# Performance work log

Measured on AMD Instinct MI355X. Metric: run time of the kernel, lower is better.

The kernel has to match this reference:

```python
import jax, jax.numpy as jnp
import numpy as np


def setup_inputs() -> dict:
    key = jax.random.key(0)
    k1, k2 = jax.random.split(key)
    batch, cw_dim = 4096, 1024
    dim_embedding, book_size = 8, 256
    dim_codes = cw_dim // dim_embedding  # 128
    x = jax.random.normal(k1, (batch, cw_dim), dtype=jnp.float32)
    codebook = jax.random.normal(k2, (dim_codes, book_size, dim_embedding), dtype=jnp.float32)
    return {"x": x, "codebook": codebook}


def reference(x, codebook):
    # Faithful JAX version of VQVAE.quantise:
    #   pairwise squared distance -> argmin -> gather embeddings -> one-hot scatter
    C, K, D = codebook.shape          # dim_codes, book_size, dim_embedding
    B = x.shape[0]
    xr = x.reshape(B, C, D)           # [B, C, D] (= view(batch*dim_codes, 1, D))
    x2 = jnp.sum(xr * xr, axis=-1)                       # [B, C]
    c2 = jnp.sum(codebook * codebook, axis=-1)           # [C, K]
    dist = x2[..., None] - 2.0 * jnp.einsum('bcd,ckd->bck', xr, codebook) + c2[None]
    idx = jnp.argmin(dist, axis=-1)                      # [B, C]
    # gather nearest codebook entry per code slot
    cw_embed = codebook[jnp.arange(C)[None, :], idx]     # [B, C, D]
    cw_embed = cw_embed.reshape(B, C * D)                # [B, cw_dim]
    # one-hot scatter of selected indices
    one_hot_idx = jax.nn.one_hot(idx, K, dtype=jnp.float32)  # [B, C, K]
    return cw_embed, one_hot_idx
```

## Files before the change

### kernel.cpp

```cpp
#include <hip/hip_runtime.h>


constexpr int B_  = 4096;
constexpr int C_  = 128;
constexpr int K_  = 256;
constexpr int D_  = 8;
constexpr int TPB = 256;

constexpr int   BPT   = 4;
constexpr int   BTILE = TPB * BPT;
constexpr float TAU2  = 1.0e-3f;

typedef float vf4 __attribute__((ext_vector_type(4)));

__device__ __forceinline__ void repair_amb(
    const float xfj[D_], int& k1j, const float s1j, const float s2j,
    const float* s_cbf, const int lane)
{
    const bool amb = (s2j - s1j) <= TAU2;
    unsigned long long mask = __ballot(amb);
    while (mask) {
        const int src = (int)__ffsll((long long)mask) - 1;
        mask &= mask - 1;
        double xd[D_];
        #pragma unroll
        for (int d = 0; d < D_; ++d) xd[d] = (double)__shfl(xfj[d], src);
        double best = 1.0e300;
        int    bk   = 0;
        #pragma unroll
        for (int t = 0; t < 4; ++t) {
            const int k = lane * 4 + t;
            const float* cv = s_cbf + k * D_;
            double cd[D_];
            #pragma unroll
            for (int d = 0; d < D_; ++d) cd[d] = (double)cv[d];
            double c2k = 0.0;
            #pragma unroll
            for (int d = 0; d < D_; ++d) c2k = fma(cd[d], cd[d], c2k);
            double dot = xd[0] * cd[0];
            #pragma unroll
            for (int d = 1; d < D_; ++d) dot = fma(xd[d], cd[d], dot);
            const double score = fma(-2.0, dot, c2k);
            if (score < best) { best = score; bk = k; }
        }
        #pragma unroll
        for (int off = 32; off >= 1; off >>= 1) {
            const double ob  = __shfl_down(best, off);
            const int    obk = __shfl_down(bk,   off);
            if (ob < best) { best = ob; bk = obk; }
        }
        const int win = __shfl(bk, 0);
        if (lane == src) k1j = win;
    }
}

__global__ __launch_bounds__(TPB) void vq_fused(
    const float* __restrict__ x,
    const float* __restrict__ cb,
    float* __restrict__ out_embed,
    float* __restrict__ out_onehot)
{
    __shared__ float s_cbf[K_ * D_];
    __shared__ float s_c2f[K_];

    const int c    = blockIdx.x;
    const int bt   = blockIdx.y;
    const int tid  = threadIdx.x;
    const int lane = tid & 63;
    const int wave = tid >> 6;

    {
        const float4* gcb = (const float4*)(cb + (size_t)c * (K_ * D_));
        ((float4*)s_cbf)[tid]       = gcb[tid];
        ((float4*)s_cbf)[tid + TPB] = gcb[tid + TPB];
    }
    __syncthreads();
    {
        const float* v = s_cbf + tid * D_;
        float s = 0.f;
        #pragma unroll
        for (int d = 0; d < D_; ++d) s = fmaf(v[d], v[d], s);
        s_c2f[tid] = s;
    }
    __syncthreads();

    const float4* scb4 = (const float4*)s_cbf;
    const int bbase = bt * BTILE;

    float xf[BPT][D_];
    #pragma unroll
    for (int j = 0; j < BPT; ++j) {
        const int b = bbase + j * TPB + tid;
        const float4* xp = (const float4*)(x + (size_t)b * (C_ * D_) + c * D_);
        const float4 a = xp[0];
        const float4 h = xp[1];
        xf[j][0] = a.x; xf[j][1] = a.y; xf[j][2] = a.z; xf[j][3] = a.w;
        xf[j][4] = h.x; xf[j][5] = h.y; xf[j][6] = h.z; xf[j][7] = h.w;
    }

    float s1[BPT], s2[BPT];
    int   k1[BPT];
    #pragma unroll
    for (int j = 0; j < BPT; ++j) { s1[j] = 3.4e38f; s2[j] = 3.4e38f; k1[j] = 0; }

    #pragma unroll 2
    for (int k = 0; k < K_; ++k) {
        const float4 clo = scb4[k * 2];
        const float4 chi = scb4[k * 2 + 1];
        const float  c2k = s_c2f[k];
        #pragma unroll
        for (int j = 0; j < BPT; ++j) {
            float dot = xf[j][0] * clo.x;
            dot = fmaf(xf[j][1], clo.y, dot);
            dot = fmaf(xf[j][2], clo.z, dot);
            dot = fmaf(xf[j][3], clo.w, dot);
            dot = fmaf(xf[j][4], chi.x, dot);
            dot = fmaf(xf[j][5], chi.y, dot);
            dot = fmaf(xf[j][6], chi.z, dot);
            dot = fmaf(xf[j][7], chi.w, dot);
            const float score = fmaf(-2.f, dot, c2k);
            s2[j] = fminf(s2[j], fmaxf(score, s1[j]));
            const bool lt = score < s1[j];
            k1[j] = lt ? k : k1[j];
            s1[j] = lt ? score : s1[j];
        }
    }

    #pragma unroll
    for (int j = 0; j < BPT; ++j) {
        repair_amb(xf[j], k1[j], s1[j], s2[j], s_cbf, lane);
    }

    #pragma unroll
    for (int j = 0; j < BPT; ++j) {
        const int    b    = bbase + j * TPB + tid;
        const size_t pair = (size_t)b * C_ + c;
        float4* dst = (float4*)(out_embed + pair * D_);
        dst[0] = ((const float4*)s_cbf)[k1[j] * 2];
        dst[1] = ((const float4*)s_cbf)[k1[j] * 2 + 1];

        const int bw = bbase + j * TPB + wave * 64;
        const int e0 = lane * 4;
        #pragma unroll 8
        for (int i = 0; i < 64; ++i) {
            const int k = __builtin_amdgcn_readlane(k1[j], i);
            vf4 v;
            v.x = (k == e0    ) ? 1.f : 0.f;
            v.y = (k == e0 + 1) ? 1.f : 0.f;
            v.z = (k == e0 + 2) ? 1.f : 0.f;
            v.w = (k == e0 + 3) ? 1.f : 0.f;
            const size_t row = (size_t)(bw + i) * C_ + c;
            ((vf4*)(out_onehot + row * K_))[lane] = v;
        }
    }
}

extern "C" void kernel_launch(void* const* d_in, const int* in_sizes, int n_in,
                              void* d_out, int out_size, void* d_ws, size_t ws_size,
                              hipStream_t stream) {
    const float* x  = (const float*)d_in[0];
    const float* cb = (const float*)d_in[1];
    float* out        = (float*)d_out;
    float* out_embed  = out;
    float* out_onehot = out + (size_t)B_ * C_ * D_;

    dim3 grid(C_, B_ / BTILE);
    vq_fused<<<grid, TPB, 0, stream>>>(x, cb, out_embed, out_onehot);
}
```

Measured before the change: 593.7 us.

## Overlap one-hot zero-fill stores with distance loop and scatter single ones afterward

The one-hot output is now zero-filled inside the codebook scan loop, one row store every other iteration, so memory writes overlap the distance compute. After the argmin, each thread writes only the single float4 holding its 1.0, after a vmcnt wait so it lands after the zeros. BPT drops from 4 to 2, which doubles the grid and matches the 128 zero-row stores to the 256 loop iterations. It relies on the wait ordering the same-address stores, and the smaller per-thread tile cuts register reuse of each codebook read.

```diff
diff --git a/kernel.cpp b/kernel.cpp
--- a/kernel.cpp
+++ b/kernel.cpp
@@ -7,7 +7,7 @@
 constexpr int D_  = 8;
 constexpr int TPB = 256;
 
-constexpr int   BPT   = 4;
+constexpr int   BPT   = 2;
 constexpr int   BTILE = TPB * BPT;
 constexpr float TAU2  = 1.0e-3f;
 
@@ -103,6 +103,8 @@
     #pragma unroll
     for (int j = 0; j < BPT; ++j) { s1[j] = 3.4e38f; s2[j] = 3.4e38f; k1[j] = 0; }
 
+    const vf4 vzero = {0.f, 0.f, 0.f, 0.f};
+
     #pragma unroll 2
     for (int k = 0; k < K_; ++k) {
         const float4 clo = scb4[k * 2];
@@ -124,6 +126,14 @@
             k1[j] = lt ? k : k1[j];
             s1[j] = lt ? score : s1[j];
         }
+        if ((k & 1) == 0) {
+            const int z  = k >> 1;
+            const int jz = z >> 6;
+            const int iz = z & 63;
+            const int bw = bbase + jz * TPB + wave * 64;
+            const size_t row = (size_t)(bw + iz) * C_ + c;
+            ((vf4*)(out_onehot + row * K_))[lane] = vzero;
+        }
     }
 
     #pragma unroll
@@ -138,20 +148,22 @@
         float4* dst = (float4*)(out_embed + pair * D_);
         dst[0] = ((const float4*)s_cbf)[k1[j] * 2];
         dst[1] = ((const float4*)s_cbf)[k1[j] * 2 + 1];
+    }
 
-        const int bw = bbase + j * TPB + wave * 64;
-        const int e0 = lane * 4;
-        #pragma unroll 8
-        for (int i = 0; i < 64; ++i) {
-            const int k = __builtin_amdgcn_readlane(k1[j], i);
-            vf4 v;
-            v.x = (k == e0    ) ? 1.f : 0.f;
-            v.y = (k == e0 + 1) ? 1.f : 0.f;
-            v.z = (k == e0 + 2) ? 1.f : 0.f;
-            v.w = (k == e0 + 3) ? 1.f : 0.f;
-            const size_t row = (size_t)(bw + i) * C_ + c;
-            ((vf4*)(out_onehot + row * K_))[lane] = v;
-        }
+    asm volatile("s_waitcnt vmcnt(0)" ::: "memory");
+
+    #pragma unroll
+    for (int j = 0; j < BPT; ++j) {
+        const int    b   = bbase + j * TPB + tid;
+        const size_t row = (size_t)b * C_ + c;
+        const int    kk  = k1[j];
+        const int    r   = kk & 3;
+        vf4 v;
+        v.x = (r == 0) ? 1.f : 0.f;
+        v.y = (r == 1) ? 1.f : 0.f;
+        v.z = (r == 2) ? 1.f : 0.f;
+        v.w = (r == 3) ? 1.f : 0.f;
+        ((vf4*)(out_onehot + row * K_))[kk >> 2] = v;
     }
 }
 
```

Measured after the change: 612.7 us. 1.03x slower.
